# Kernel optimization log

Hardware: AMD Instinct MI355X
Metric: run time of the kernel (lower is better)

Reference implementation:

```python
import jax, jax.numpy as jnp
import numpy as np
from math import factorial, pi, sqrt

LMAX = 5
MUL_IN = 128
NUM_CHANNELS = 4
NUM_RADII = 20
RES_BETA = 180
RES_ALPHA = 359
IRREPS_DIM = (LMAX + 1) ** 2  # 36
NUM_GRAPHS = 32
NUM_SPECIES = 5


def _sh_grid_matrix():
    """Real spherical harmonics evaluated on a Gauss-Legendre (beta) x uniform (alpha) grid.

    Returns Y of shape [RES_BETA, RES_ALPHA, IRREPS_DIM]; this is the dense form of
    e3nn's to_s2grid (Legendre x Fourier) transform matrix.
    """
    y, _ = np.polynomial.legendre.leggauss(RES_BETA)  # y = cos(beta), quadrature='gausslegendre'
    alpha = 2.0 * np.pi * np.arange(RES_ALPHA) / RES_ALPHA
    # Associated Legendre P_l^m(y) (no Condon-Shortley), shape [l, m, RES_BETA]
    P = np.zeros((LMAX + 1, LMAX + 1, RES_BETA))
    P[0, 0] = 1.0
    sy = np.sqrt(np.maximum(1.0 - y * y, 0.0))
    for m in range(1, LMAX + 1):
        P[m, m] = (2 * m - 1) * sy * P[m - 1, m - 1]
    for m in range(LMAX):
        P[m + 1, m] = (2 * m + 1) * y * P[m, m]
    for m in range(LMAX + 1):
        for l in range(m + 2, LMAX + 1):
            P[l, m] = ((2 * l - 1) * y * P[l - 1, m] - (l + m - 1) * P[l - 2, m]) / (l - m)
    Y = np.zeros((RES_BETA, RES_ALPHA, IRREPS_DIM))
    idx = 0
    for l in range(LMAX + 1):
        for m in range(-l, l + 1):
            am = abs(m)
            K = sqrt((2 * l + 1) / (4.0 * pi) * factorial(l - am) / factorial(l + am))
            if m == 0:
                Y[:, :, idx] = (K * P[l, 0])[:, None]
            elif m > 0:
                Y[:, :, idx] = sqrt(2.0) * K * P[l, m][:, None] * np.cos(m * alpha)[None, :]
            else:
                Y[:, :, idx] = sqrt(2.0) * K * P[l, am][:, None] * np.sin(am * alpha)[None, :]
            idx += 1
    return Y.astype(np.float32)


def setup_inputs() -> dict:
    key = jax.random.key(0)
    k1, k2, k3, k4 = jax.random.split(key, 4)
    focus = jax.random.normal(k1, (NUM_GRAPHS, MUL_IN * IRREPS_DIM), dtype=jnp.float32)
    embed_table = jax.random.normal(k2, (NUM_SPECIES, MUL_IN * (LMAX + 1)), dtype=jnp.float32)
    linear_weights = jax.random.normal(k3, (LMAX + 1, MUL_IN, NUM_RADII * NUM_CHANNELS), dtype=jnp.float32)
    target_species = jax.random.randint(k4, (NUM_GRAPHS,), 0, NUM_SPECIES)
    return {
        "focus_node_embeddings": focus,
        "embed_table": embed_table,
        "linear_weights": linear_weights,
        "target_species": target_species,
    }


def reference(focus_node_embeddings, embed_table, linear_weights, target_species):
    G = focus_node_embeddings.shape[0]
    Y = jnp.asarray(_sh_grid_matrix())  # [B, A, 36]
    emb = embed_table[target_species]  # [G, num_irreps = 768], one scalar per irrep channel
    inv_sqrt_fan = 1.0 / np.sqrt(MUL_IN).astype(np.float32)

    coeffs = []
    off_in, off_emb = 0, 0
    for l in range(LMAX + 1):
        dim_m = 2 * l + 1
        # irreps-block view: [G, mul_in, 2l+1]
        x_l = focus_node_embeddings[:, off_in:off_in + MUL_IN * dim_m].reshape(G, MUL_IN, dim_m)
        # per-irrep scalar gating (target_species_embeddings * focus_node_embeddings)
        x_l = x_l * emb[:, off_emb:off_emb + MUL_IN, None]
        # equivariant Linear: mixes multiplicities only, per m, fan-in normalized
        y_l = jnp.einsum("gim,io->gom", x_l, linear_weights[l]) * inv_sqrt_fan
        # mul_to_axis(num_channels) then mul_to_axis(num_radii)
        coeffs.append(y_l.reshape(G, NUM_CHANNELS, NUM_RADII, dim_m))
        off_in += MUL_IN * dim_m
        off_emb += MUL_IN
    position_coeffs = jnp.concatenate(coeffs, axis=-1)  # [G, C, R, 36]

    # to_s2grid: coefficients -> spherical grid signal
    grid = jnp.einsum("gcri,bai->gcrba", position_coeffs, Y)  # [G, C, R, B, A]
    # logsumexp over channels, then max-normalize per graph
    logits = jax.scipy.special.logsumexp(grid, axis=1)  # [G, R, B, A]
    logits = logits - logits.max(axis=(-3, -2, -1), keepdims=True)
    return position_coeffs, logits
```

## Files before the change

### kernel.cpp

```cpp
#include <hip/hip_runtime.h>

#define G_N    32
#define MUL    128
#define RADII  20
#define CH     4
#define RES_B  180
#define RES_A  359
#define IDIM   36
#define COEFF_N (G_N*CH*RADII*IDIM)
#define PER_G   (RADII*RES_B*RES_A)
#define PER_G4  (PER_G/4)

typedef float v2f __attribute__((ext_vector_type(2)));

__device__ __forceinline__ float fexp2(float x){
#if __has_builtin(__builtin_amdgcn_exp2f)
  return __builtin_amdgcn_exp2f(x);
#else
  return exp2f(x);
#endif
}
__device__ __forceinline__ float flog2(float x){
#if __has_builtin(__builtin_amdgcn_logf)
  return __builtin_amdgcn_logf(x);
#else
  return log2f(x);
#endif
}
__device__ __forceinline__ unsigned enc_f(float f){
  unsigned u = __float_as_uint(f);
  return (u & 0x80000000u) ? ~u : (u | 0x80000000u);
}
__device__ __forceinline__ float dec_f(unsigned k){
  return __uint_as_float((k & 0x80000000u) ? (k ^ 0x80000000u) : ~k);
}

__global__ void setup_kernel(float* __restrict__ PYs, float* __restrict__ Ftab){
  const double PI = 3.14159265358979323846;
  const double LOG2E = 1.4426950408889634074;
  __shared__ double ak[RES_B + 1], bk[RES_B + 1];
  int t = threadIdx.x;
  if (t >= 2 && t <= RES_B){
    ak[t] = (2.0*t - 1.0) / (double)t;
    bk[t] = (t - 1.0) / (double)t;
  }
  __syncthreads();
  if (t < RES_B){
    int i = RES_B - 1 - t;
    double x = cos(PI * (i + 0.75) / (RES_B + 0.5));
    for (int it = 0; it < 5; ++it){
      double p0 = 1.0, p1 = x;
      for (int k = 2; k <= RES_B; ++k){
        double t1 = ak[k] * x;
        double pk = fma(t1, p1, -(bk[k] * p0));
        p0 = p1; p1 = pk;
      }
      x -= p1 * (x*x - 1.0) / ((double)RES_B * (x*p1 - p0));
    }
    double y = x;
    double sy = sqrt(fmax(1.0 - y*y, 0.0));
    double P[6][6];
    P[0][0] = 1.0;
    for (int m = 1; m < 6; ++m) P[m][m] = (2.0*m - 1.0)*sy*P[m-1][m-1];
    for (int m = 0; m < 5; ++m) P[m+1][m] = (2.0*m + 1.0)*y*P[m][m];
    for (int m = 0; m < 6; ++m)
      for (int l = m + 2; l < 6; ++l)
        P[l][m] = ((2.0*l - 1.0)*y*P[l-1][m] - (l + m - 1.0)*P[l-2][m]) / (double)(l - m);
    const double fact[11] = {1,1,2,6,24,120,720,5040,40320,362880,3628800};
    for (int l = 0; l < 6; ++l)
      for (int m = 0; m <= l; ++m){
        double K = sqrt((2.0*l + 1.0)/(4.0*PI)*fact[l-m]/fact[l+m]);
        double v = K * P[l][m] * LOG2E;
        if (m > 0) v *= sqrt(2.0);
        PYs[t*36 + l*6 + m] = (float)v;
      }
  } else if (t < RES_B + RES_A){
    int a = t - RES_B;
    double al = 2.0*PI*a/(double)RES_A;
    Ftab[a*12 + 0] = 1.0f;
    for (int m = 1; m <= 5; ++m){
      Ftab[a*12 + m]     = (float)cos(m*al);
      Ftab[a*12 + 5 + m] = (float)sin(m*al);
    }
    Ftab[a*12 + 11] = 0.f;
  }
}

__global__ void coeffs_kernel(const float* __restrict__ focus, const float* __restrict__ embt,
                              const float* __restrict__ W, const int* __restrict__ tspec,
                              float* __restrict__ out){
  int idx = blockIdx.x * 256 + threadIdx.x;
  if (idx >= COEFF_N) return;
  int i36 = idx % IDIM;
  int go  = idx / IDIM;
  int o   = go % (CH*RADII);
  int g   = go / (CH*RADII);
  int l   = (int)sqrtf((float)i36 + 0.5f);
  int mo  = i36 - l*l;
  int dim = 2*l + 1;
  const float* fp = focus + g*(MUL*IDIM) + MUL*l*l + mo;
  const float* ep = embt + tspec[g]*(MUL*6) + MUL*l;
  const float* wp = W + l*(MUL*80) + o;
  float s = 0.f;
  #pragma unroll 4
  for (int i = 0; i < MUL; ++i)
    s = fmaf(fp[i*dim] * ep[i], wp[i*80], s);
  out[idx] = s * 0.088388347648318447f;
}

__global__ __launch_bounds__(192) void compute_kernel(const float* __restrict__ coeffs,
                          const float* __restrict__ PYs, const float* __restrict__ Ftab,
                          float* __restrict__ out, unsigned* __restrict__ gmax){
  const int BCH = 45;
  int blk   = blockIdx.x;
  int chunk = blk & 3;
  int gr    = blk >> 2;
  int r = gr % RADII;
  int g = gr / RADII;
  int tid = threadIdx.x;
  int b0  = chunk * BCH;

  __shared__ float cv[CH][IDIM];
  __shared__ __align__(16) float tmpa[BCH][12][4];
  __shared__ float wred[3];

  if (tid < CH*IDIM){
    int c = tid / IDIM, i = tid % IDIM;
    cv[c][i] = coeffs[((g*CH + c)*RADII + r)*IDIM + i];
  }
  float fr[11];
  if (tid < 180){
    #pragma unroll
    for (int k = 0; k < 11; ++k) fr[k] = Ftab[tid*12 + k];
  }
  __syncthreads();

  for (int v = tid; v < BCH*44; v += 192){
    int bl = v / 44, cm = v % 44;
    int c = cm / 11, mm = cm % 11;
    int am, ii;
    if (mm == 0)      { am = 0;      ii = 0;        }
    else if (mm <= 5) { am = mm;     ii = mm;       }
    else              { am = mm - 5; ii = -(mm-5);  }
    const float* py = PYs + (b0 + bl)*36 + am;
    float s = 0.f;
    for (int l = am; l < 6; ++l)
      s = fmaf(cv[c][l*l + l + ii], py[l*6], s);
    tmpa[bl][mm][c] = s;
  }
  __syncthreads();

  float bmax = -INFINITY;
  if (tid < 180){
    float* pp = out + ((size_t)(g*RADII + r)*RES_B + b0)*RES_A + tid;
    float* pm = pp + (359 - 2*tid);
    for (int bl = 0; bl < BCH; ++bl){
      const float4* tq = reinterpret_cast<const float4*>(&tmpa[bl][0][0]);
      float4 q0 = tq[0];
      v2f C01 = {q0.x, q0.y}, C23 = {q0.z, q0.w};
      #pragma unroll
      for (int mm = 1; mm <= 5; ++mm){
        float4 q = tq[mm];
        v2f fs = {fr[mm], fr[mm]};
        v2f a01 = {q.x, q.y}, a23 = {q.z, q.w};
        C01 = __builtin_elementwise_fma(a01, fs, C01);
        C23 = __builtin_elementwise_fma(a23, fs, C23);
      }
      float4 q6 = tq[6];
      v2f f6 = {fr[6], fr[6]};
      v2f S01 = (v2f){q6.x, q6.y} * f6, S23 = (v2f){q6.z, q6.w} * f6;
      #pragma unroll
      for (int mm = 7; mm <= 10; ++mm){
        float4 q = tq[mm];
        v2f fs = {fr[mm], fr[mm]};
        v2f a01 = {q.x, q.y}, a23 = {q.z, q.w};
        S01 = __builtin_elementwise_fma(a01, fs, S01);
        S23 = __builtin_elementwise_fma(a23, fs, S23);
      }
      v2f hp01 = C01 + S01, hp23 = C23 + S23;
      v2f hm01 = C01 - S01, hm23 = C23 - S23;
      float sp = (fexp2(hp01.x) + fexp2(hp01.y)) + (fexp2(hp23.x) + fexp2(hp23.y));
      float sm = (fexp2(hm01.x) + fexp2(hm01.y)) + (fexp2(hm23.x) + fexp2(hm23.y));
      float lgp = flog2(sp);
      float lgm = flog2(sm);
      *pp = lgp;
      if (tid) *pm = lgm;
      bmax = fmaxf(bmax, fmaxf(lgp, lgm));
      pp += RES_A; pm += RES_A;
    }
  }
  #pragma unroll
  for (int off = 32; off > 0; off >>= 1)
    bmax = fmaxf(bmax, __shfl_xor(bmax, off, 64));
  int lane = tid & 63, w = tid >> 6;
  if (lane == 0) wred[w] = bmax;
  __syncthreads();
  if (tid == 0){
    float m = fmaxf(wred[0], fmaxf(wred[1], wred[2]));
    atomicMax(gmax + g, enc_f(m));
  }
}

__global__ __launch_bounds__(256) void fixup_kernel(float* __restrict__ logits,
                                                    const unsigned* __restrict__ gmax){
  const float LN2 = 0.69314718055994531f;
  const int total4 = G_N * PER_G4;
  float4* l4 = reinterpret_cast<float4*>(logits);
  int stride = gridDim.x * 256;
  for (int i = blockIdx.x * 256 + threadIdx.x; i < total4; i += stride){
    int g = (int)(((unsigned)i) / PER_G4);
    float nsub = -dec_f(gmax[g]) * LN2;
    float4 v = l4[i];
    v.x = fmaf(v.x, LN2, nsub); v.y = fmaf(v.y, LN2, nsub);
    v.z = fmaf(v.z, LN2, nsub); v.w = fmaf(v.w, LN2, nsub);
    l4[i] = v;
  }
}

extern "C" void kernel_launch(void* const* d_in, const int* in_sizes, int n_in,
                              void* d_out, int out_size, void* d_ws, size_t ws_size,
                              hipStream_t stream){
  const float* focus = (const float*)d_in[0];
  const float* embt  = (const float*)d_in[1];
  const float* W     = (const float*)d_in[2];
  const int*   tspec = (const int*)d_in[3];
  float* out = (float*)d_out;
  float* ws  = (float*)d_ws;
  unsigned* gmax = (unsigned*)d_ws;
  float* PYs  = ws + 32;
  float* Ftab = ws + 32 + RES_B*36;

  hipMemsetAsync(d_ws, 0, 128, stream);
  setup_kernel<<<1, 576, 0, stream>>>(PYs, Ftab);
  coeffs_kernel<<<(COEFF_N + 255)/256, 256, 0, stream>>>(focus, embt, W, tspec, out);
  float* logits = out + COEFF_N;
  compute_kernel<<<G_N*RADII*4, 192, 0, stream>>>(out, PYs, Ftab, logits, gmax);
  fixup_kernel<<<2048, 256, 0, stream>>>(logits, gmax);
}
```

Measured before the change: 174.6 us.

## Precompute beta-Legendre partial sums in a separate kernel and defer log2 to fixup

Moves the per-beta Legendre contraction out of compute_kernel into a new tmp_kernel that writes a [G,R,B,44] buffer to workspace. compute_kernel then reads those values straight from global memory with a wave-uniform pointer and drops its shared staging and one barrier. It now stores the sum of exponentials instead of its log and takes the max of that, with log2 applied in the fixup pass. This trims work on the compute kernel's critical path, at the cost of an extra launch and a round trip of about 4 MB through global memory. Since log is monotonic the max is unchanged, but the positive sums could overflow where the logs would not.

Measured after the change: 270.2 us. 1.55x slower.

```diff
diff --git a/kernel.cpp b/kernel.cpp
--- a/kernel.cpp
+++ b/kernel.cpp
@@ -10,6 +10,7 @@
 #define COEFF_N (G_N*CH*RADII*IDIM)
 #define PER_G   (RADII*RES_B*RES_A)
 #define PER_G4  (PER_G/4)
+#define TMP_N   (G_N*RADII*RES_B*44)
 
 typedef float v2f __attribute__((ext_vector_type(2)));
 
@@ -108,54 +109,58 @@
   out[idx] = s * 0.088388347648318447f;
 }
 
-__global__ __launch_bounds__(192) void compute_kernel(const float* __restrict__ coeffs,
-                          const float* __restrict__ PYs, const float* __restrict__ Ftab,
+__global__ void tmp_kernel(const float* __restrict__ coeffs, const float* __restrict__ PYs,
+                           float* __restrict__ tmp){
+  int idx = blockIdx.x * 256 + threadIdx.x;
+  if (idx >= TMP_N) return;
+  int c    = idx & 3;
+  int mm   = (idx >> 2) % 11;
+  int t    = idx / 44;
+  int beta = t % RES_B;
+  int gr   = t / RES_B;
+  int g = gr / RADII, r = gr % RADII;
+  int am, ii;
+  if (mm == 0)      { am = 0;      ii = 0;        }
+  else if (mm <= 5) { am = mm;     ii = mm;       }
+  else              { am = mm - 5; ii = -(mm-5);  }
+  const float* py  = PYs + beta*36 + am;
+  const float* cvp = coeffs + ((size_t)((g*CH + c)*RADII + r))*IDIM;
+  float s = 0.f;
+  for (int l = am; l < 6; ++l)
+    s = fmaf(cvp[l*l + l + ii], py[l*6], s);
+  tmp[idx] = s;
+}
+
+__global__ __launch_bounds__(192) void compute_kernel(const float* __restrict__ tmp,
+                          const float* __restrict__ Ftab,
                           float* __restrict__ out, unsigned* __restrict__ gmax){
   const int BCH = 45;
   int blk   = blockIdx.x;
   int chunk = blk & 3;
   int gr    = blk >> 2;
-  int r = gr % RADII;
-  int g = gr / RADII;
   int tid = threadIdx.x;
   int b0  = chunk * BCH;
 
-  __shared__ float cv[CH][IDIM];
-  __shared__ __align__(16) float tmpa[BCH][12][4];
   __shared__ float wred[3];
 
-  if (tid < CH*IDIM){
-    int c = tid / IDIM, i = tid % IDIM;
-    cv[c][i] = coeffs[((g*CH + c)*RADII + r)*IDIM + i];
-  }
+  const float* tb = tmp + ((size_t)gr*RES_B + b0)*44;
+  {
+    uintptr_t p = (uintptr_t)tb;
+    unsigned lo = __builtin_amdgcn_readfirstlane((unsigned)p);
+    unsigned hi = __builtin_amdgcn_readfirstlane((unsigned)(p >> 32));
+    tb = (const float*)(((uintptr_t)hi << 32) | lo);
+  }
+
   float fr[11];
+  #pragma unroll
+  for (int k = 0; k < 11; ++k) fr[k] = Ftab[tid*12 + k];
+
+  float smax = 0.f;
   if (tid < 180){
-    #pragma unroll
-    for (int k = 0; k < 11; ++k) fr[k] = Ftab[tid*12 + k];
-  }
-  __syncthreads();
-
-  for (int v = tid; v < BCH*44; v += 192){
-    int bl = v / 44, cm = v % 44;
-    int c = cm / 11, mm = cm % 11;
-    int am, ii;
-    if (mm == 0)      { am = 0;      ii = 0;        }
-    else if (mm <= 5) { am = mm;     ii = mm;       }
-    else              { am = mm - 5; ii = -(mm-5);  }
-    const float* py = PYs + (b0 + bl)*36 + am;
-    float s = 0.f;
-    for (int l = am; l < 6; ++l)
-      s = fmaf(cv[c][l*l + l + ii], py[l*6], s);
-    tmpa[bl][mm][c] = s;
-  }
-  __syncthreads();
-
-  float bmax = -INFINITY;
-  if (tid < 180){
-    float* pp = out + ((size_t)(g*RADII + r)*RES_B + b0)*RES_A + tid;
+    float* pp = out + ((size_t)gr*RES_B + b0)*RES_A + tid;
     float* pm = pp + (359 - 2*tid);
     for (int bl = 0; bl < BCH; ++bl){
-      const float4* tq = reinterpret_cast<const float4*>(&tmpa[bl][0][0]);
+      const float4* tq = reinterpret_cast<const float4*>(tb + bl*44);
       float4 q0 = tq[0];
       v2f C01 = {q0.x, q0.y}, C23 = {q0.z, q0.w};
       #pragma unroll
@@ -181,23 +186,21 @@
       v2f hm01 = C01 - S01, hm23 = C23 - S23;
       float sp = (fexp2(hp01.x) + fexp2(hp01.y)) + (fexp2(hp23.x) + fexp2(hp23.y));
       float sm = (fexp2(hm01.x) + fexp2(hm01.y)) + (fexp2(hm23.x) + fexp2(hm23.y));
-      float lgp = flog2(sp);
-      float lgm = flog2(sm);
-      *pp = lgp;
-      if (tid) *pm = lgm;
-      bmax = fmaxf(bmax, fmaxf(lgp, lgm));
+      *pp = sp;
+      if (tid) *pm = sm;
+      smax = fmaxf(smax, fmaxf(sp, sm));
       pp += RES_A; pm += RES_A;
     }
   }
   #pragma unroll
   for (int off = 32; off > 0; off >>= 1)
-    bmax = fmaxf(bmax, __shfl_xor(bmax, off, 64));
+    smax = fmaxf(smax, __shfl_xor(smax, off, 64));
   int lane = tid & 63, w = tid >> 6;
-  if (lane == 0) wred[w] = bmax;
+  if (lane == 0) wred[w] = smax;
   __syncthreads();
   if (tid == 0){
     float m = fmaxf(wred[0], fmaxf(wred[1], wred[2]));
-    atomicMax(gmax + g, enc_f(m));
+    atomicMax(gmax + gr/RADII, enc_f(m));
   }
 }
 
@@ -209,10 +212,12 @@
   int stride = gridDim.x * 256;
   for (int i = blockIdx.x * 256 + threadIdx.x; i < total4; i += stride){
     int g = (int)(((unsigned)i) / PER_G4);
-    float nsub = -dec_f(gmax[g]) * LN2;
+    float nsub = -flog2(dec_f(gmax[g])) * LN2;
     float4 v = l4[i];
-    v.x = fmaf(v.x, LN2, nsub); v.y = fmaf(v.y, LN2, nsub);
-    v.z = fmaf(v.z, LN2, nsub); v.w = fmaf(v.w, LN2, nsub);
+    v.x = fmaf(flog2(v.x), LN2, nsub);
+    v.y = fmaf(flog2(v.y), LN2, nsub);
+    v.z = fmaf(flog2(v.z), LN2, nsub);
+    v.w = fmaf(flog2(v.w), LN2, nsub);
     l4[i] = v;
   }
 }
@@ -229,11 +234,13 @@
   unsigned* gmax = (unsigned*)d_ws;
   float* PYs  = ws + 32;
   float* Ftab = ws + 32 + RES_B*36;
+  float* tmp  = ws + 16384;
 
   hipMemsetAsync(d_ws, 0, 128, stream);
   setup_kernel<<<1, 576, 0, stream>>>(PYs, Ftab);
   coeffs_kernel<<<(COEFF_N + 255)/256, 256, 0, stream>>>(focus, embt, W, tspec, out);
+  tmp_kernel<<<(TMP_N + 255)/256, 256, 0, stream>>>(out, PYs, tmp);
   float* logits = out + COEFF_N;
-  compute_kernel<<<G_N*RADII*4, 192, 0, stream>>>(out, PYs, Ftab, logits, gmax);
+  compute_kernel<<<G_N*RADII*4, 192, 0, stream>>>(tmp, Ftab, logits, gmax);
   fixup_kernel<<<2048, 256, 0, stream>>>(logits, gmax);
 }
```

## Use single-wave blocks for grid compute and defer log2 to the fixup pass

Applied to the files above, without the earlier changes.

The compute kernel now runs one 64-thread wavefront per block. Each thread handles three alpha columns and reuses the shared-memory row coefficients, which it loads into registers once per beta row. This removes the cross-wave LDS reduction and the idle lanes in the third wave. The kernel now stores the raw sum of exponentials, and the fixup pass applies log2 along with the max normalization, so the transcendental work moves into a kernel that was already memory bound. The trade-offs are more register pressure and a larger share of threads idle in the shared-memory fill phase.

After: 189.4 us. 8.4% more time.

```diff
diff --git a/kernel.cpp b/kernel.cpp
--- a/kernel.cpp
+++ b/kernel.cpp
@@ -108,7 +108,7 @@
   out[idx] = s * 0.088388347648318447f;
 }
 
-__global__ __launch_bounds__(192) void compute_kernel(const float* __restrict__ coeffs,
+__global__ __launch_bounds__(64) void compute_kernel(const float* __restrict__ coeffs,
                           const float* __restrict__ PYs, const float* __restrict__ Ftab,
                           float* __restrict__ out, unsigned* __restrict__ gmax){
   const int BCH = 45;
@@ -122,20 +122,21 @@
 
   __shared__ float cv[CH][IDIM];
   __shared__ __align__(16) float tmpa[BCH][12][4];
-  __shared__ float wred[3];
-
-  if (tid < CH*IDIM){
-    int c = tid / IDIM, i = tid % IDIM;
+
+  for (int v = tid; v < CH*IDIM; v += 64){
+    int c = v / IDIM, i = v % IDIM;
     cv[c][i] = coeffs[((g*CH + c)*RADII + r)*IDIM + i];
   }
-  float fr[11];
-  if (tid < 180){
-    #pragma unroll
-    for (int k = 0; k < 11; ++k) fr[k] = Ftab[tid*12 + k];
+  float f0[11], f1[11], f2[11];
+  #pragma unroll
+  for (int k = 0; k < 11; ++k){
+    f0[k] = Ftab[tid*12 + k];
+    f1[k] = Ftab[(tid+64)*12 + k];
+    f2[k] = Ftab[(tid+128)*12 + k];
   }
   __syncthreads();
 
-  for (int v = tid; v < BCH*44; v += 192){
+  for (int v = tid; v < BCH*44; v += 64){
     int bl = v / 44, cm = v % 44;
     int c = cm / 11, mm = cm % 11;
     int am, ii;
@@ -150,55 +151,48 @@
   }
   __syncthreads();
 
-  float bmax = -INFINITY;
-  if (tid < 180){
-    float* pp = out + ((size_t)(g*RADII + r)*RES_B + b0)*RES_A + tid;
-    float* pm = pp + (359 - 2*tid);
-    for (int bl = 0; bl < BCH; ++bl){
-      const float4* tq = reinterpret_cast<const float4*>(&tmpa[bl][0][0]);
-      float4 q0 = tq[0];
-      v2f C01 = {q0.x, q0.y}, C23 = {q0.z, q0.w};
+  float smax = 0.f;
+  float* row = out + ((size_t)gr*RES_B + b0)*RES_A;
+  for (int bl = 0; bl < BCH; ++bl){
+    const float4* tq = reinterpret_cast<const float4*>(&tmpa[bl][0][0]);
+    float4 q[11];
+    #pragma unroll
+    for (int mm = 0; mm < 11; ++mm) q[mm] = tq[mm];
+    #pragma unroll
+    for (int k = 0; k < 3; ++k){
+      if (k == 2 && tid >= 52) break;
+      const float* fr = (k == 0) ? f0 : (k == 1) ? f1 : f2;
+      int p = tid + 64*k;
+      v2f C01 = {q[0].x, q[0].y}, C23 = {q[0].z, q[0].w};
       #pragma unroll
       for (int mm = 1; mm <= 5; ++mm){
-        float4 q = tq[mm];
         v2f fs = {fr[mm], fr[mm]};
-        v2f a01 = {q.x, q.y}, a23 = {q.z, q.w};
-        C01 = __builtin_elementwise_fma(a01, fs, C01);
-        C23 = __builtin_elementwise_fma(a23, fs, C23);
-      }
-      float4 q6 = tq[6];
+        C01 = __builtin_elementwise_fma((v2f){q[mm].x, q[mm].y}, fs, C01);
+        C23 = __builtin_elementwise_fma((v2f){q[mm].z, q[mm].w}, fs, C23);
+      }
       v2f f6 = {fr[6], fr[6]};
-      v2f S01 = (v2f){q6.x, q6.y} * f6, S23 = (v2f){q6.z, q6.w} * f6;
+      v2f S01 = (v2f){q[6].x, q[6].y} * f6, S23 = (v2f){q[6].z, q[6].w} * f6;
       #pragma unroll
       for (int mm = 7; mm <= 10; ++mm){
-        float4 q = tq[mm];
         v2f fs = {fr[mm], fr[mm]};
-        v2f a01 = {q.x, q.y}, a23 = {q.z, q.w};
-        S01 = __builtin_elementwise_fma(a01, fs, S01);
-        S23 = __builtin_elementwise_fma(a23, fs, S23);
+        S01 = __builtin_elementwise_fma((v2f){q[mm].x, q[mm].y}, fs, S01);
+        S23 = __builtin_elementwise_fma((v2f){q[mm].z, q[mm].w}, fs, S23);
       }
       v2f hp01 = C01 + S01, hp23 = C23 + S23;
       v2f hm01 = C01 - S01, hm23 = C23 - S23;
       float sp = (fexp2(hp01.x) + fexp2(hp01.y)) + (fexp2(hp23.x) + fexp2(hp23.y));
       float sm = (fexp2(hm01.x) + fexp2(hm01.y)) + (fexp2(hm23.x) + fexp2(hm23.y));
-      float lgp = flog2(sp);
-      float lgm = flog2(sm);
-      *pp = lgp;
-      if (tid) *pm = lgm;
-      bmax = fmaxf(bmax, fmaxf(lgp, lgm));
-      pp += RES_A; pm += RES_A;
+      row[p] = sp;
+      if (p) row[359 - p] = sm;
+      smax = fmaxf(smax, fmaxf(sp, sm));
     }
+    row += RES_A;
   }
   #pragma unroll
   for (int off = 32; off > 0; off >>= 1)
-    bmax = fmaxf(bmax, __shfl_xor(bmax, off, 64));
-  int lane = tid & 63, w = tid >> 6;
-  if (lane == 0) wred[w] = bmax;
-  __syncthreads();
-  if (tid == 0){
-    float m = fmaxf(wred[0], fmaxf(wred[1], wred[2]));
-    atomicMax(gmax + g, enc_f(m));
-  }
+    smax = fmaxf(smax, __shfl_xor(smax, off, 64));
+  if (tid == 0)
+    atomicMax(gmax + g, enc_f(smax));
 }
 
 __global__ __launch_bounds__(256) void fixup_kernel(float* __restrict__ logits,
@@ -209,10 +203,12 @@
   int stride = gridDim.x * 256;
   for (int i = blockIdx.x * 256 + threadIdx.x; i < total4; i += stride){
     int g = (int)(((unsigned)i) / PER_G4);
-    float nsub = -dec_f(gmax[g]) * LN2;
+    float nsub = -flog2(dec_f(gmax[g])) * LN2;
     float4 v = l4[i];
-    v.x = fmaf(v.x, LN2, nsub); v.y = fmaf(v.y, LN2, nsub);
-    v.z = fmaf(v.z, LN2, nsub); v.w = fmaf(v.w, LN2, nsub);
+    v.x = fmaf(flog2(v.x), LN2, nsub);
+    v.y = fmaf(flog2(v.y), LN2, nsub);
+    v.z = fmaf(flog2(v.z), LN2, nsub);
+    v.w = fmaf(flog2(v.w), LN2, nsub);
     l4[i] = v;
   }
 }
@@ -234,6 +230,6 @@
   setup_kernel<<<1, 576, 0, stream>>>(PYs, Ftab);
   coeffs_kernel<<<(COEFF_N + 255)/256, 256, 0, stream>>>(focus, embt, W, tspec, out);
   float* logits = out + COEFF_N;
-  compute_kernel<<<G_N*RADII*4, 192, 0, stream>>>(out, PYs, Ftab, logits, gmax);
+  compute_kernel<<<G_N*RADII*4, 64, 0, stream>>>(out, PYs, Ftab, logits, gmax);
   fixup_kernel<<<2048, 256, 0, stream>>>(logits, gmax);
 }
```
